# Performance work log

Hardware: AMD Instinct MI355X
Metric: run time of the kernel (lower is better)

The kernel has to match this reference:

```python
import jax, jax.numpy as jnp
import numpy as np

D_MODEL = 1024
N_HEADS = 16
HEAD_DIM = D_MODEL // N_HEADS


def setup_inputs() -> dict:
    key = jax.random.key(0)
    kx, kq, kk, kv, ko = jax.random.split(key, 5)
    B, T = 2, 2048
    # nn.Linear(d_model, d_model, bias=False) weights, stored as [out, in] like torch
    s = 1.0 / np.sqrt(D_MODEL)
    x = jax.random.normal(kx, (B, T, D_MODEL), dtype=jnp.float32)
    Wq = jax.random.uniform(kq, (D_MODEL, D_MODEL), minval=-s, maxval=s, dtype=jnp.float32)
    Wk = jax.random.uniform(kk, (D_MODEL, D_MODEL), minval=-s, maxval=s, dtype=jnp.float32)
    Wv = jax.random.uniform(kv, (D_MODEL, D_MODEL), minval=-s, maxval=s, dtype=jnp.float32)
    Wo = jax.random.uniform(ko, (D_MODEL, D_MODEL), minval=-s, maxval=s, dtype=jnp.float32)
    return {"x": x, "Wq": Wq, "Wk": Wk, "Wv": Wv, "Wo": Wo}


def reference(x, Wq, Wk, Wv, Wo):
    B, T, C = x.shape
    H, Dh = N_HEADS, HEAD_DIM
    # projections (torch Linear: x @ W.T)
    q = (x @ Wq.T).reshape(B, T, H, Dh).transpose(0, 2, 1, 3)  # [B,H,T,Dh]
    k = (x @ Wk.T).reshape(B, T, H, Dh).transpose(0, 2, 1, 3)
    v = (x @ Wv.T).reshape(B, T, H, Dh).transpose(0, 2, 1, 3)
    scores = jnp.einsum('bhqd,bhkd->bhqk', q, k) / jnp.sqrt(jnp.float32(Dh))
    causal = jnp.tril(jnp.ones((T, T), dtype=bool))  # [T,T]
    scores = jnp.where(causal[None, None], scores, -jnp.inf)
    attn = jax.nn.softmax(scores, axis=-1)
    out = jnp.einsum('bhqk,bhkd->bhqd', attn, v)  # [B,H,T,Dh]
    out = out.transpose(0, 2, 1, 3).reshape(B, T, C)
    return out @ Wo.T
```

## Files before the change

### kernel.cpp

```cpp
#include <hip/hip_runtime.h>
#include <hip/hip_bf16.h>

#define BB 2
#define TT 2048
#define CC 1024
#define HH 16
#define DH 64

typedef __attribute__((ext_vector_type(8))) short bf16x8;
typedef __attribute__((ext_vector_type(4))) float f32x4;
typedef __attribute__((ext_vector_type(16))) float f32x16;
using bf16 = __hip_bfloat16;
using u32 = unsigned int;

union cvt8u { bf16x8 v; bf16 b[8]; };

__device__ __forceinline__ bf16x8 load8(const bf16* p) {
    return *reinterpret_cast<const bf16x8*>(p);
}

__device__ __forceinline__ bf16x8 cvt8f(const float* p) {
    const float4 a = *reinterpret_cast<const float4*>(p);
    const float4 c = *reinterpret_cast<const float4*>(p + 4);
    cvt8u u;
    u.b[0] = __float2bfloat16(a.x); u.b[1] = __float2bfloat16(a.y);
    u.b[2] = __float2bfloat16(a.z); u.b[3] = __float2bfloat16(a.w);
    u.b[4] = __float2bfloat16(c.x); u.b[5] = __float2bfloat16(c.y);
    u.b[6] = __float2bfloat16(c.z); u.b[7] = __float2bfloat16(c.w);
    return u.v;
}

__device__ __forceinline__ f32x4 mfma16(bf16x8 a, bf16x8 b, f32x4 c) {
    return __builtin_amdgcn_mfma_f32_16x16x32_bf16(a, b, c, 0, 0, 0);
}

__device__ __forceinline__ f32x16 mfma32(bf16x8 a, bf16x8 b, f32x16 c) {
    return __builtin_amdgcn_mfma_f32_32x32x16_bf16(a, b, c, 0, 0, 0);
}

__device__ __forceinline__ u32 pk2(float lo, float hi) {
    union { bf16 b; unsigned short u; } a, c;
    a.b = __float2bfloat16(lo);
    c.b = __float2bfloat16(hi);
    return (u32)a.u | ((u32)c.u << 16);
}

__device__ __forceinline__ void gload_lds16(const bf16* g, bf16* l) {
    __builtin_amdgcn_global_load_lds(
        (const __attribute__((address_space(1))) void*)g,
        (__attribute__((address_space(3))) void*)l, 16, 0, 0);
}

#define QSCALE (0.125f * 1.44269504088896f)


__global__ __launch_bounds__(256) void cvt_x(const float* __restrict__ in,
                                             bf16* __restrict__ out) {
    const int i = blockIdx.x * 256 + threadIdx.x;
    *(reinterpret_cast<bf16x8*>(out) + i) = cvt8f(in + (size_t)i * 8);
}

__global__ __launch_bounds__(256) void cvt4_w(const float* __restrict__ w0,
                                              const float* __restrict__ w1,
                                              const float* __restrict__ w2,
                                              const float* __restrict__ w3,
                                              bf16* __restrict__ out) {
    const float* in = (blockIdx.y == 0) ? w0 : (blockIdx.y == 1) ? w1
                    : (blockIdx.y == 2) ? w2 : w3;
    const int i = blockIdx.x * 256 + threadIdx.x;
    bf16* o = out + (size_t)blockIdx.y * CC * CC;
    *(reinterpret_cast<bf16x8*>(o) + i) = cvt8f(in + (size_t)i * 8);
}

template <int MODE>
__global__ __launch_bounds__(256) void gemm3(const bf16* __restrict__ A,
                                             const bf16* __restrict__ B,
                                             bf16* __restrict__ oq,
                                             bf16* __restrict__ ok,
                                             bf16* __restrict__ ov,
                                             float* __restrict__ outf) {
    __shared__ __align__(16) bf16 As[128 * 32];
    __shared__ __align__(16) bf16 Bs[128 * 32];
    const int lane = threadIdx.x & 63;
    const int wv = threadIdx.x >> 6;
    const int l15 = lane & 15;
    const int g = lane >> 4;
    const int m0 = blockIdx.x * 128;
    const int n0 = blockIdx.y * 128;

    const int srow = wv * 16 + (lane >> 2);
    const int skg = (lane & 3) * 8;
    const bf16* gA0 = A + (size_t)(m0 + srow) * CC + skg;
    const bf16* gA1 = A + (size_t)(m0 + 64 + srow) * CC + skg;
    const bf16* gB0 = B + (size_t)(n0 + srow) * CC + skg;
    const bf16* gB1 = B + (size_t)(n0 + 64 + srow) * CC + skg;
    bf16* lA0 = As + wv * 512;
    bf16* lA1 = As + 2048 + wv * 512;
    bf16* lB0 = Bs + wv * 512;
    bf16* lB1 = Bs + 2048 + wv * 512;

    const int mw = (wv >> 1) * 64;
    const int nw = (wv & 1) * 64;

    f32x4 acc[4][4] = {};

    for (int kk = 0; kk < CC; kk += 32) {
        __syncthreads();
        gload_lds16(gA0 + kk, lA0);
        gload_lds16(gA1 + kk, lA1);
        gload_lds16(gB0 + kk, lB0);
        gload_lds16(gB1 + kk, lB1);
        __syncthreads();

        bf16x8 af[4], wf[4];
#pragma unroll
        for (int mi = 0; mi < 4; mi++)
            af[mi] = load8(As + (mw + mi * 16 + l15) * 32 + g * 8);
#pragma unroll
        for (int ni = 0; ni < 4; ni++)
            wf[ni] = load8(Bs + (nw + ni * 16 + l15) * 32 + g * 8);
#pragma unroll
        for (int mi = 0; mi < 4; mi++)
#pragma unroll
            for (int ni = 0; ni < 4; ni++)
                acc[mi][ni] = mfma16(af[mi], wf[ni], acc[mi][ni]);
    }

#pragma unroll
    for (int mi = 0; mi < 4; mi++) {
#pragma unroll
        for (int ni = 0; ni < 4; ni++) {
            const int n = n0 + nw + ni * 16 + l15;
#pragma unroll
            for (int r = 0; r < 4; r++) {
                const int m = m0 + mw + mi * 16 + g * 4 + r;
                const float v = acc[mi][ni][r];
                if (MODE == 1) {
                    outf[(size_t)m * CC + n] = v;
                } else {
                    const int b = m >> 11, t = m & (TT - 1);
                    const int mat = n >> 10, nn = n & 1023;
                    const int h = nn >> 6, d = nn & 63;
                    if (mat == 0) {
                        oq[((size_t)((b * HH + h) * TT + t) << 6) + d] = __float2bfloat16(v * QSCALE);
                    } else if (mat == 1) {
                        ok[((size_t)((b * HH + h) * TT + t) << 6) + d] = __float2bfloat16(v);
                    } else {
                        ov[(size_t)((b * HH + h) * DH + d) * TT + ((t + (d << 6)) & (TT - 1))] = __float2bfloat16(v);
                    }
                }
            }
        }
    }
}

template <int MODE>
__global__ __launch_bounds__(256) void gemm2(const bf16* __restrict__ A,
                                             const float* __restrict__ W0,
                                             const float* __restrict__ W1,
                                             const float* __restrict__ W2,
                                             bf16* __restrict__ oq,
                                             bf16* __restrict__ ok,
                                             bf16* __restrict__ ov,
                                             float* __restrict__ outf) {
    const int lane = threadIdx.x & 63;
    const int wv = threadIdx.x >> 6;
    const int l15 = lane & 15;
    const int g = lane >> 4;
    const int mw = blockIdx.x * 128 + (wv >> 1) * 64;
    const int nw = blockIdx.y * 128 + (wv & 1) * 64;

    f32x4 acc[4][4] = {};

    const bf16* ap[4];
#pragma unroll
    for (int mi = 0; mi < 4; mi++)
        ap[mi] = A + (size_t)(mw + mi * 16 + l15) * CC + g * 8;

    const float* wfp[4];
#pragma unroll
    for (int ni = 0; ni < 4; ni++) {
        const int nt = nw + ni * 16;
        const float* base = (MODE == 1) ? W0
                          : (nt < 1024) ? W0 : (nt < 2048) ? W1 : W2;
        wfp[ni] = base + (size_t)((nt & 1023) + l15) * CC + g * 8;
    }

#pragma unroll 2
    for (int kk = 0; kk < CC; kk += 32) {
        bf16x8 af[4], wf[4];
#pragma unroll
        for (int mi = 0; mi < 4; mi++) af[mi] = load8(ap[mi] + kk);
#pragma unroll
        for (int ni = 0; ni < 4; ni++) wf[ni] = cvt8f(wfp[ni] + kk);
#pragma unroll
        for (int mi = 0; mi < 4; mi++)
#pragma unroll
            for (int ni = 0; ni < 4; ni++)
                acc[mi][ni] = mfma16(af[mi], wf[ni], acc[mi][ni]);
    }

#pragma unroll
    for (int mi = 0; mi < 4; mi++) {
#pragma unroll
        for (int ni = 0; ni < 4; ni++) {
            const int n = nw + ni * 16 + l15;
#pragma unroll
            for (int r = 0; r < 4; r++) {
                const int m = mw + mi * 16 + g * 4 + r;
                const float v = acc[mi][ni][r];
                if (MODE == 1) {
                    outf[(size_t)m * CC + n] = v;
                } else {
                    const int b = m >> 11, t = m & (TT - 1);
                    const int mat = n >> 10, nn = n & 1023;
                    const int h = nn >> 6, d = nn & 63;
                    if (mat == 0) {
                        oq[((size_t)((b * HH + h) * TT + t) << 6) + d] = __float2bfloat16(v * QSCALE);
                    } else if (mat == 1) {
                        ok[((size_t)((b * HH + h) * TT + t) << 6) + d] = __float2bfloat16(v);
                    } else {
                        ov[(size_t)((b * HH + h) * DH + d) * TT + ((t + (d << 6)) & (TT - 1))] = __float2bfloat16(v);
                    }
                }
            }
        }
    }
}

__global__ __launch_bounds__(128, 2) void attn_v14(const bf16* __restrict__ Q,
                                                   const bf16* __restrict__ K,
                                                   const bf16* __restrict__ Vt,
                                                   bf16* __restrict__ out) {
    __shared__ __align__(64) float o_cmb[2][64][16];
    __shared__ float l_cmb[32];

    const int lane = threadIdx.x & 63;
    const int wv = threadIdx.x >> 6;
    const int l31 = lane & 31;
    const int hh = lane >> 5;

    const int bid = blockIdx.x;
    const int xcd = bid & 7;
    const int idx = bid >> 3;
    const int bh = xcd * 4 + (idx >> 6);
    const int c = 63 - (idx & 63);
    const int qb = c * 32;

    const bf16* Qh = Q + (size_t)bh * TT * DH;
    const bf16* Kh = K + (size_t)bh * TT * DH;
    const bf16* Vh = Vt + (size_t)bh * DH * TT;

    bf16x8 qf[4];
#pragma unroll
    for (int dc = 0; dc < 4; dc++)
        qf[dc] = load8(Qh + (size_t)(qb + l31) * DH + dc * 16 + hh * 8);

    f32x16 o0 = {}, o1 = {};
    float l_part = 0.0f;

    const int qlane = qb + l31;
    const int d0 = l31, d1 = 32 + l31;
    const int s0 = d0 << 6, s1 = d1 << 6;

    bf16x8 kf[4], vf00, vf01, vf10, vf11;
    {
        const int k0 = wv * 32;
#pragma unroll
        for (int dc = 0; dc < 4; dc++)
            kf[dc] = load8(Kh + (size_t)(k0 + l31) * DH + dc * 16 + hh * 8);
        vf00 = load8(Vh + (size_t)d0 * TT + ((k0 + hh * 8 + s0) & (TT - 1)));
        vf01 = load8(Vh + (size_t)d0 * TT + ((k0 + 16 + hh * 8 + s0) & (TT - 1)));
        vf10 = load8(Vh + (size_t)d1 * TT + ((k0 + hh * 8 + s1) & (TT - 1)));
        vf11 = load8(Vh + (size_t)d1 * TT + ((k0 + 16 + hh * 8 + s1) & (TT - 1)));
    }

    for (int kb = wv; kb <= c; kb += 2) {
        const int k0 = kb * 32;
        const bool more = (kb + 2 <= c);

        bf16x8 kfn[4], vn00, vn01, vn10, vn11;
        if (more) {
            const int kn = k0 + 64;
#pragma unroll
            for (int dc = 0; dc < 4; dc++)
                kfn[dc] = load8(Kh + (size_t)(kn + l31) * DH + dc * 16 + hh * 8);
            vn00 = load8(Vh + (size_t)d0 * TT + ((kn + hh * 8 + s0) & (TT - 1)));
            vn01 = load8(Vh + (size_t)d0 * TT + ((kn + 16 + hh * 8 + s0) & (TT - 1)));
            vn10 = load8(Vh + (size_t)d1 * TT + ((kn + hh * 8 + s1) & (TT - 1)));
            vn11 = load8(Vh + (size_t)d1 * TT + ((kn + 16 + hh * 8 + s1) & (TT - 1)));
        }

        f32x16 S = {};
#pragma unroll
        for (int dc = 0; dc < 4; dc++) S = mfma32(kf[dc], qf[dc], S);

        if (kb == c) {
#pragma unroll
            for (int r = 0; r < 16; r++) {
                const int c_r = (r & 3) + 8 * (r >> 2);
                if (k0 + c_r + 4 * hh > qlane) S[r] = -1e30f;
            }
        }

        float e[16];
#pragma unroll
        for (int r = 0; r < 16; r++) {
            e[r] = exp2f(S[r]);
            l_part += e[r];
        }

        u32 w0 = pk2(e[0], e[1]),   w1 = pk2(e[2], e[3]);
        u32 w2 = pk2(e[4], e[5]),   w3 = pk2(e[6], e[7]);
        u32 w4 = pk2(e[8], e[9]),   w5 = pk2(e[10], e[11]);
        u32 w6 = pk2(e[12], e[13]), w7 = pk2(e[14], e[15]);
        const u32 x0 = __shfl_xor(w0, 32), x1 = __shfl_xor(w1, 32);
        const u32 x2 = __shfl_xor(w2, 32), x3 = __shfl_xor(w3, 32);
        const u32 x4 = __shfl_xor(w4, 32), x5 = __shfl_xor(w5, 32);
        const u32 x6 = __shfl_xor(w6, 32), x7 = __shfl_xor(w7, 32);

        union { u32 u[4]; bf16x8 v; } a1, a2;
        a1.u[0] = hh ? x2 : w0;  a1.u[1] = hh ? x3 : w1;
        a1.u[2] = hh ? w2 : x0;  a1.u[3] = hh ? w3 : x1;
        a2.u[0] = hh ? x6 : w4;  a2.u[1] = hh ? x7 : w5;
        a2.u[2] = hh ? w6 : x4;  a2.u[3] = hh ? w7 : x5;

        o0 = mfma32(a1.v, vf00, o0);
        o0 = mfma32(a2.v, vf01, o0);
        o1 = mfma32(a1.v, vf10, o1);
        o1 = mfma32(a2.v, vf11, o1);

        if (more) {
#pragma unroll
            for (int dc = 0; dc < 4; dc++) kf[dc] = kfn[dc];
            vf00 = vn00; vf01 = vn01; vf10 = vn10; vf11 = vn11;
        }
    }

    l_part += __shfl_xor(l_part, 32);

    if (wv == 1) {
        *reinterpret_cast<f32x16*>(&o_cmb[0][lane][0]) = o0;
        *reinterpret_cast<f32x16*>(&o_cmb[1][lane][0]) = o1;
        if (lane < 32) l_cmb[lane] = l_part;
    }
    __syncthreads();
    if (wv == 1) return;

    o0 += *reinterpret_cast<const f32x16*>(&o_cmb[0][lane][0]);
    o1 += *reinterpret_cast<const f32x16*>(&o_cmb[1][lane][0]);
    const float linv = 1.0f / (l_part + l_cmb[l31]);

    const int b = bh >> 4, h = bh & 15;
#pragma unroll
    for (int r = 0; r < 16; r++) {
        const int qrow = (r & 3) + 8 * (r >> 2) + 4 * hh;
        const float inv = __shfl(linv, qrow);
        const int t = qb + qrow;
        bf16* op = out + (size_t)(b * TT + t) * CC + h * DH;
        op[l31] = __float2bfloat16(o0[r] * inv);
        op[32 + l31] = __float2bfloat16(o1[r] * inv);
    }
}

extern "C" void kernel_launch(void* const* d_in, const int* in_sizes, int n_in,
                              void* d_out, int out_size, void* d_ws, size_t ws_size,
                              hipStream_t stream) {
    const float* x  = (const float*)d_in[0];
    const float* Wq = (const float*)d_in[1];
    const float* Wk = (const float*)d_in[2];
    const float* Wv = (const float*)d_in[3];
    const float* Wo = (const float*)d_in[4];
    float* out = (float*)d_out;

    const size_t per = (size_t)BB * HH * TT * DH;
    bf16* Qws  = (bf16*)d_ws;
    bf16* Kws  = Qws + per;
    bf16* Vtws = Kws + per;
    bf16* xbf  = Vtws + per;
    bf16* attn = xbf;
    bf16* Wball = attn + per;
    const bool full = ws_size >= 5 * per * sizeof(bf16);

    const dim3 blk(256);
    cvt_x<<<dim3(2048), blk, 0, stream>>>(x, xbf);

    if (full) {
        cvt4_w<<<dim3(512, 4), blk, 0, stream>>>(Wq, Wk, Wv, Wo, Wball);
        gemm3<0><<<dim3(32, 24), blk, 0, stream>>>(
            xbf, Wball, Qws, Kws, Vtws, nullptr);
    } else {
        gemm2<0><<<dim3(32, 24), blk, 0, stream>>>(
            xbf, Wq, Wk, Wv, Qws, Kws, Vtws, nullptr);
    }

    attn_v14<<<dim3(2048), dim3(128), 0, stream>>>(Qws, Kws, Vtws, attn);

    if (full) {
        gemm3<1><<<dim3(32, 8), blk, 0, stream>>>(
            attn, Wball + (size_t)3 * CC * CC, nullptr, nullptr, nullptr, out);
    } else {
        gemm2<1><<<dim3(32, 8), blk, 0, stream>>>(
            attn, Wo, nullptr, nullptr, nullptr, nullptr, nullptr, out);
    }
}
```

Measured before the change: 221.8 us.

## Process two 32-row query tiles per attention block to reuse K/V loads

Each attention block now handles 64 query rows as two 32-row tiles that share every K and V fragment loaded from global memory, which halves the grid to 1024 blocks. The intent is to cut redundant K/V global traffic and amortise load latency over twice the MFMA work. s_setprio hints are also added around the MFMA sections. The cost is higher register pressure from doubled accumulators and Q fragments, plus a larger shared-memory combine buffer, which may lower occupancy under launch_bounds(128,2).

```diff
diff --git a/kernel.cpp b/kernel.cpp
--- a/kernel.cpp
+++ b/kernel.cpp
@@ -228,12 +228,12 @@
     }
 }
 
-__global__ __launch_bounds__(128, 2) void attn_v14(const bf16* __restrict__ Q,
+__global__ __launch_bounds__(128, 2) void attn_v16(const bf16* __restrict__ Q,
                                                    const bf16* __restrict__ K,
                                                    const bf16* __restrict__ Vt,
                                                    bf16* __restrict__ out) {
-    __shared__ __align__(64) float o_cmb[2][64][16];
-    __shared__ float l_cmb[32];
+    __shared__ __align__(64) float o_cmb[2][2][64][16];
+    __shared__ float l_cmb[2][32];
 
     const int lane = threadIdx.x & 63;
     const int wv = threadIdx.x >> 6;
@@ -243,23 +243,28 @@
     const int bid = blockIdx.x;
     const int xcd = bid & 7;
     const int idx = bid >> 3;
-    const int bh = xcd * 4 + (idx >> 6);
-    const int c = 63 - (idx & 63);
-    const int qb = c * 32;
+    const int bh = xcd * 4 + (idx >> 5);
+    const int c = 31 - (idx & 31);
+    const int qbA = c * 64;
+    const int qbB = c * 64 + 32;
+    const int kbmax = 2 * c + 1;
 
     const bf16* Qh = Q + (size_t)bh * TT * DH;
     const bf16* Kh = K + (size_t)bh * TT * DH;
     const bf16* Vh = Vt + (size_t)bh * DH * TT;
 
-    bf16x8 qf[4];
-#pragma unroll
-    for (int dc = 0; dc < 4; dc++)
-        qf[dc] = load8(Qh + (size_t)(qb + l31) * DH + dc * 16 + hh * 8);
-
-    f32x16 o0 = {}, o1 = {};
-    float l_part = 0.0f;
-
-    const int qlane = qb + l31;
+    bf16x8 qfA[4], qfB[4];
+#pragma unroll
+    for (int dc = 0; dc < 4; dc++) {
+        qfA[dc] = load8(Qh + (size_t)(qbA + l31) * DH + dc * 16 + hh * 8);
+        qfB[dc] = load8(Qh + (size_t)(qbB + l31) * DH + dc * 16 + hh * 8);
+    }
+
+    f32x16 oA0 = {}, oA1 = {}, oB0 = {}, oB1 = {};
+    float lA = 0.0f, lB = 0.0f;
+
+    const int qlaneA = qbA + l31;
+    const int qlaneB = qbB + l31;
     const int d0 = l31, d1 = 32 + l31;
     const int s0 = d0 << 6, s1 = d1 << 6;
 
@@ -275,9 +280,10 @@
         vf11 = load8(Vh + (size_t)d1 * TT + ((k0 + 16 + hh * 8 + s1) & (TT - 1)));
     }
 
-    for (int kb = wv; kb <= c; kb += 2) {
+    for (int kb = wv; kb <= kbmax; kb += 2) {
         const int k0 = kb * 32;
-        const bool more = (kb + 2 <= c);
+        const bool more = (kb + 2 <= kbmax);
+        const bool actA = (kb <= 2 * c);
 
         bf16x8 kfn[4], vn00, vn01, vn10, vn11;
         if (more) {
@@ -291,44 +297,86 @@
             vn11 = load8(Vh + (size_t)d1 * TT + ((kn + 16 + hh * 8 + s1) & (TT - 1)));
         }
 
-        f32x16 S = {};
-#pragma unroll
-        for (int dc = 0; dc < 4; dc++) S = mfma32(kf[dc], qf[dc], S);
-
-        if (kb == c) {
+        f32x16 SA = {}, SB = {};
+        __builtin_amdgcn_s_setprio(1);
+        if (actA) {
+#pragma unroll
+            for (int dc = 0; dc < 4; dc++) SA = mfma32(kf[dc], qfA[dc], SA);
+        }
+#pragma unroll
+        for (int dc = 0; dc < 4; dc++) SB = mfma32(kf[dc], qfB[dc], SB);
+        __builtin_amdgcn_s_setprio(0);
+
+        if (kb == 2 * c) {
 #pragma unroll
             for (int r = 0; r < 16; r++) {
                 const int c_r = (r & 3) + 8 * (r >> 2);
-                if (k0 + c_r + 4 * hh > qlane) S[r] = -1e30f;
-            }
-        }
-
-        float e[16];
-#pragma unroll
-        for (int r = 0; r < 16; r++) {
-            e[r] = exp2f(S[r]);
-            l_part += e[r];
-        }
-
-        u32 w0 = pk2(e[0], e[1]),   w1 = pk2(e[2], e[3]);
-        u32 w2 = pk2(e[4], e[5]),   w3 = pk2(e[6], e[7]);
-        u32 w4 = pk2(e[8], e[9]),   w5 = pk2(e[10], e[11]);
-        u32 w6 = pk2(e[12], e[13]), w7 = pk2(e[14], e[15]);
-        const u32 x0 = __shfl_xor(w0, 32), x1 = __shfl_xor(w1, 32);
-        const u32 x2 = __shfl_xor(w2, 32), x3 = __shfl_xor(w3, 32);
-        const u32 x4 = __shfl_xor(w4, 32), x5 = __shfl_xor(w5, 32);
-        const u32 x6 = __shfl_xor(w6, 32), x7 = __shfl_xor(w7, 32);
-
-        union { u32 u[4]; bf16x8 v; } a1, a2;
-        a1.u[0] = hh ? x2 : w0;  a1.u[1] = hh ? x3 : w1;
-        a1.u[2] = hh ? w2 : x0;  a1.u[3] = hh ? w3 : x1;
-        a2.u[0] = hh ? x6 : w4;  a2.u[1] = hh ? x7 : w5;
-        a2.u[2] = hh ? w6 : x4;  a2.u[3] = hh ? w7 : x5;
-
-        o0 = mfma32(a1.v, vf00, o0);
-        o0 = mfma32(a2.v, vf01, o0);
-        o1 = mfma32(a1.v, vf10, o1);
-        o1 = mfma32(a2.v, vf11, o1);
+                if (k0 + c_r + 4 * hh > qlaneA) SA[r] = -1e30f;
+            }
+        }
+        if (kb == kbmax) {
+#pragma unroll
+            for (int r = 0; r < 16; r++) {
+                const int c_r = (r & 3) + 8 * (r >> 2);
+                if (k0 + c_r + 4 * hh > qlaneB) SB[r] = -1e30f;
+            }
+        }
+
+        if (actA) {
+            float e[16];
+#pragma unroll
+            for (int r = 0; r < 16; r++) {
+                e[r] = exp2f(SA[r]);
+                lA += e[r];
+            }
+            u32 w0 = pk2(e[0], e[1]),   w1 = pk2(e[2], e[3]);
+            u32 w2 = pk2(e[4], e[5]),   w3 = pk2(e[6], e[7]);
+            u32 w4 = pk2(e[8], e[9]),   w5 = pk2(e[10], e[11]);
+            u32 w6 = pk2(e[12], e[13]), w7 = pk2(e[14], e[15]);
+            const u32 x0 = __shfl_xor(w0, 32), x1 = __shfl_xor(w1, 32);
+            const u32 x2 = __shfl_xor(w2, 32), x3 = __shfl_xor(w3, 32);
+            const u32 x4 = __shfl_xor(w4, 32), x5 = __shfl_xor(w5, 32);
+            const u32 x6 = __shfl_xor(w6, 32), x7 = __shfl_xor(w7, 32);
+            union { u32 u[4]; bf16x8 v; } a1, a2;
+            a1.u[0] = hh ? x2 : w0;  a1.u[1] = hh ? x3 : w1;
+            a1.u[2] = hh ? w2 : x0;  a1.u[3] = hh ? w3 : x1;
+            a2.u[0] = hh ? x6 : w4;  a2.u[1] = hh ? x7 : w5;
+            a2.u[2] = hh ? w6 : x4;  a2.u[3] = hh ? w7 : x5;
+            __builtin_amdgcn_s_setprio(1);
+            oA0 = mfma32(a1.v, vf00, oA0);
+            oA0 = mfma32(a2.v, vf01, oA0);
+            oA1 = mfma32(a1.v, vf10, oA1);
+            oA1 = mfma32(a2.v, vf11, oA1);
+            __builtin_amdgcn_s_setprio(0);
+        }
+
+        {
+            float e[16];
+#pragma unroll
+            for (int r = 0; r < 16; r++) {
+                e[r] = exp2f(SB[r]);
+                lB += e[r];
+            }
+            u32 w0 = pk2(e[0], e[1]),   w1 = pk2(e[2], e[3]);
+            u32 w2 = pk2(e[4], e[5]),   w3 = pk2(e[6], e[7]);
+            u32 w4 = pk2(e[8], e[9]),   w5 = pk2(e[10], e[11]);
+            u32 w6 = pk2(e[12], e[13]), w7 = pk2(e[14], e[15]);
+            const u32 x0 = __shfl_xor(w0, 32), x1 = __shfl_xor(w1, 32);
+            const u32 x2 = __shfl_xor(w2, 32), x3 = __shfl_xor(w3, 32);
+            const u32 x4 = __shfl_xor(w4, 32), x5 = __shfl_xor(w5, 32);
+            const u32 x6 = __shfl_xor(w6, 32), x7 = __shfl_xor(w7, 32);
+            union { u32 u[4]; bf16x8 v; } a1, a2;
+            a1.u[0] = hh ? x2 : w0;  a1.u[1] = hh ? x3 : w1;
+            a1.u[2] = hh ? w2 : x0;  a1.u[3] = hh ? w3 : x1;
+            a2.u[0] = hh ? x6 : w4;  a2.u[1] = hh ? x7 : w5;
+            a2.u[2] = hh ? w6 : x4;  a2.u[3] = hh ? w7 : x5;
+            __builtin_amdgcn_s_setprio(1);
+            oB0 = mfma32(a1.v, vf00, oB0);
+            oB0 = mfma32(a2.v, vf01, oB0);
+            oB1 = mfma32(a1.v, vf10, oB1);
+            oB1 = mfma32(a2.v, vf11, oB1);
+            __builtin_amdgcn_s_setprio(0);
+        }
 
         if (more) {
 #pragma unroll
@@ -337,29 +385,41 @@
         }
     }
 
-    l_part += __shfl_xor(l_part, 32);
+    lA += __shfl_xor(lA, 32);
+    lB += __shfl_xor(lB, 32);
 
     if (wv == 1) {
-        *reinterpret_cast<f32x16*>(&o_cmb[0][lane][0]) = o0;
-        *reinterpret_cast<f32x16*>(&o_cmb[1][lane][0]) = o1;
-        if (lane < 32) l_cmb[lane] = l_part;
+        *reinterpret_cast<f32x16*>(&o_cmb[0][0][lane][0]) = oA0;
+        *reinterpret_cast<f32x16*>(&o_cmb[0][1][lane][0]) = oA1;
+        *reinterpret_cast<f32x16*>(&o_cmb[1][0][lane][0]) = oB0;
+        *reinterpret_cast<f32x16*>(&o_cmb[1][1][lane][0]) = oB1;
+        if (lane < 32) {
+            l_cmb[0][lane] = lA;
+            l_cmb[1][lane] = lB;
+        }
     }
     __syncthreads();
     if (wv == 1) return;
 
-    o0 += *reinterpret_cast<const f32x16*>(&o_cmb[0][lane][0]);
-    o1 += *reinterpret_cast<const f32x16*>(&o_cmb[1][lane][0]);
-    const float linv = 1.0f / (l_part + l_cmb[l31]);
+    oA0 += *reinterpret_cast<const f32x16*>(&o_cmb[0][0][lane][0]);
+    oA1 += *reinterpret_cast<const f32x16*>(&o_cmb[0][1][lane][0]);
+    oB0 += *reinterpret_cast<const f32x16*>(&o_cmb[1][0][lane][0]);
+    oB1 += *reinterpret_cast<const f32x16*>(&o_cmb[1][1][lane][0]);
+    const float linvA = 1.0f / (lA + l_cmb[0][l31]);
+    const float linvB = 1.0f / (lB + l_cmb[1][l31]);
 
     const int b = bh >> 4, h = bh & 15;
 #pragma unroll
     for (int r = 0; r < 16; r++) {
         const int qrow = (r & 3) + 8 * (r >> 2) + 4 * hh;
-        const float inv = __shfl(linv, qrow);
-        const int t = qb + qrow;
-        bf16* op = out + (size_t)(b * TT + t) * CC + h * DH;
-        op[l31] = __float2bfloat16(o0[r] * inv);
-        op[32 + l31] = __float2bfloat16(o1[r] * inv);
+        const float invA = __shfl(linvA, qrow);
+        const float invB = __shfl(linvB, qrow);
+        bf16* opA = out + (size_t)(b * TT + qbA + qrow) * CC + h * DH;
+        bf16* opB = out + (size_t)(b * TT + qbB + qrow) * CC + h * DH;
+        opA[l31] = __float2bfloat16(oA0[r] * invA);
+        opA[32 + l31] = __float2bfloat16(oA1[r] * invA);
+        opB[l31] = __float2bfloat16(oB0[r] * invB);
+        opB[32 + l31] = __float2bfloat16(oB1[r] * invB);
     }
 }
 
@@ -394,7 +454,7 @@
             xbf, Wq, Wk, Wv, Qws, Kws, Vtws, nullptr);
     }
 
-    attn_v14<<<dim3(2048), dim3(128), 0, stream>>>(Qws, Kws, Vtws, attn);
+    attn_v16<<<dim3(1024), dim3(128), 0, stream>>>(Qws, Kws, Vtws, attn);
 
     if (full) {
         gemm3<1><<<dim3(32, 8), blk, 0, stream>>>(
```

After: 214.3 us. 1.03x faster.
